# Kernel optimization log

Hardware: AMD Instinct MI355X
Metric: run time of the kernel (lower is better)

Reference implementation:

```python
import jax, jax.numpy as jnp
import numpy as np

B, C, H, W = 8, 256, 64, 64
CQ = C // 8  # q/k projection dim = 32


def setup_inputs() -> dict:
    key = jax.random.key(0)
    ks = jax.random.split(key, 8)
    sq = 1.0 / np.sqrt(C)
    return {
        "x": jax.random.normal(ks[0], (B, C, H, W), dtype=jnp.float32),
        "wq": jax.random.normal(ks[1], (CQ, C), dtype=jnp.float32) * sq,
        "bq": jax.random.normal(ks[2], (CQ,), dtype=jnp.float32) * 0.01,
        "wk": jax.random.normal(ks[3], (CQ, C), dtype=jnp.float32) * sq,
        "bk": jax.random.normal(ks[4], (CQ,), dtype=jnp.float32) * 0.01,
        "wv": jax.random.normal(ks[5], (C, C), dtype=jnp.float32) * sq,
        "bv": jax.random.normal(ks[6], (C,), dtype=jnp.float32) * 0.01,
        "gamma": jax.random.normal(ks[7], (1,), dtype=jnp.float32) * 0.1,
    }


def reference(x, wq, bq, wk, bk, wv, bv, gamma):
    b, c, h, w = x.shape
    n = h * w
    xf = x.reshape(b, c, n)  # [b, C, N] (1x1 conv == channel matmul)
    q = jnp.einsum('oc,bcn->bno', wq, xf) + bq  # [b, N, Cq]
    k = jnp.einsum('oc,bcn->bon', wk, xf) + bk[None, :, None]  # [b, Cq, N]
    v = jnp.einsum('oc,bcn->bon', wv, xf) + bv[None, :, None]  # [b, C, N]
    energy = jnp.einsum('bnq,bqm->bnm', q, k)  # [b, N, N]
    attn = jax.nn.softmax(energy, axis=-1)
    # out[b,c,i] = sum_j v[b,c,j] * attn[b,i,j]  (bmm(v, attn^T))
    out = jnp.einsum('bcj,bij->bci', v, attn).reshape(b, c, h, w)
    return gamma[0] * out + x
```

## Files before the change

kernel.cpp:

```cpp
#include <hip/hip_runtime.h>
#include <hip/hip_bf16.h>
#include <stdint.h>

#define CC 256
#define CQD 32
#define NND 4096

typedef __bf16 bf16x8 __attribute__((ext_vector_type(8)));
typedef float f32x4 __attribute__((ext_vector_type(4)));
typedef float f32x16 __attribute__((ext_vector_type(16)));

__device__ __forceinline__ bf16x8 ld_bf16x8(const __bf16* p) {
    return *reinterpret_cast<const bf16x8*>(p);
}

__global__ __launch_bounds__(256) void prep_weights(
    const float* __restrict__ wq, const float* __restrict__ wk,
    const float* __restrict__ wv, __bf16* __restrict__ wqkb,
    __bf16* __restrict__ wvb) {
    int i = blockIdx.x * 256 + threadIdx.x;
    if (i < 32 * 256) {
        wqkb[i] = (__bf16)wq[i];
    } else if (i < 64 * 256) {
        wqkb[i] = (__bf16)wk[i - 32 * 256];
    } else {
        int j = i - 64 * 256;
        if (j < 256 * 256) wvb[j] = (__bf16)wv[j];
    }
}

__global__ __launch_bounds__(256, 4) void proj_qkv(
    const float* __restrict__ x, const __bf16* __restrict__ wqkb,
    const __bf16* __restrict__ wvb, const float* __restrict__ bq,
    const float* __restrict__ bk, const float* __restrict__ bv,
    __bf16* __restrict__ qb, __bf16* __restrict__ kb,
    __bf16* __restrict__ vb) {
    __shared__ __align__(16) __bf16 xt[32 * 256];
    __shared__ __align__(16) __bf16 wt[320 * 32];

    const int blk = blockIdx.x;
    const int b = blk & 7;
    const int n0 = (blk >> 3) * 32;
    const int tid = threadIdx.x;
    const int lane = tid & 63;
    const int w = tid >> 6;

    const __bf16* wsrc = wqkb + (size_t)(lane >> 2) * CC + (lane & 3) * 8;

#pragma unroll
    for (int i = 0; i < 5; i++) {
        int ins = w * 5 + i;
        __builtin_amdgcn_global_load_lds(
            (const __attribute__((address_space(1))) void*)(wsrc + (size_t)ins * 16 * CC),
            (__attribute__((address_space(3))) void*)(&wt[ins * 512]), 16, 0, 0);
    }

    {
        const int cl = tid >> 3;
        const int ng = tid & 7;
        const float* xrow = x + (size_t)b * CC * NND + n0 + ng * 4;
        f32x4 xv[8];
#pragma unroll
        for (int p = 0; p < 8; p++)
            xv[p] = *reinterpret_cast<const f32x4*>(xrow + (size_t)(p * 32 + cl) * NND);
#pragma unroll
        for (int p = 0; p < 8; p++) {
            int c = p * 32 + cl;
            int c8 = c >> 3;
#pragma unroll
            for (int j = 0; j < 4; j++) {
                int row = ng * 4 + j;
                xt[row * 256 + ((c8 ^ (row & 7)) * 8) + (c & 7)] = (__bf16)xv[p][j];
            }
        }
    }
    __syncthreads();

    const int l15 = lane & 15;
    const int quad = lane >> 4;
    const f32x4 fzero = {0.f, 0.f, 0.f, 0.f};
    f32x4 aqk[2];
    f32x4 av[4][2];
#pragma unroll
    for (int i = 0; i < 2; i++) aqk[i] = fzero;
#pragma unroll
    for (int i = 0; i < 4; i++)
#pragma unroll
        for (int j = 0; j < 2; j++) av[i][j] = fzero;

#pragma unroll
    for (int t = 0; t < 8; t++) {
        const int k0 = t * 32;
        bf16x8 bfx[2];
#pragma unroll
        for (int nt = 0; nt < 2; nt++) {
            int row = nt * 16 + l15;
            int g = (k0 >> 3) + quad;
            bfx[nt] = ld_bf16x8(&xt[row * 256 + ((g ^ (row & 7)) * 8)]);
        }
        bf16x8 aqf = ld_bf16x8(&wt[(w * 16 + l15) * 32 + quad * 8]);
        bf16x8 avf[4];
#pragma unroll
        for (int mt = 0; mt < 4; mt++)
            avf[mt] = ld_bf16x8(&wt[(64 + (w * 4 + mt) * 16 + l15) * 32 + quad * 8]);
        asm volatile("s_waitcnt lgkmcnt(0)" ::: "memory");
        __builtin_amdgcn_s_barrier();
        int kn = (k0 + 32) & 255;
#pragma unroll
        for (int i = 0; i < 5; i++) {
            int ins = w * 5 + i;
            __builtin_amdgcn_global_load_lds(
                (const __attribute__((address_space(1))) void*)(wsrc + (size_t)ins * 16 * CC + kn),
                (__attribute__((address_space(3))) void*)(&wt[ins * 512]), 16, 0, 0);
        }
#pragma unroll
        for (int nt = 0; nt < 2; nt++)
            aqk[nt] = __builtin_amdgcn_mfma_f32_16x16x32_bf16(aqf, bfx[nt], aqk[nt], 0, 0, 0);
#pragma unroll
        for (int mt = 0; mt < 4; mt++)
#pragma unroll
            for (int nt = 0; nt < 2; nt++)
                av[mt][nt] = __builtin_amdgcn_mfma_f32_16x16x32_bf16(avf[mt], bfx[nt], av[mt][nt], 0, 0, 0);
        asm volatile("s_waitcnt vmcnt(0)" ::: "memory");
        __builtin_amdgcn_s_barrier();
    }

    {
        const int ob = (w & 1) * 16 + quad * 4;
        const float* bias = (w < 2) ? bq : bk;
        __bf16* base = (w < 2) ? qb : kb;
#pragma unroll
        for (int nt = 0; nt < 2; nt++) {
            int n = n0 + nt * 16 + l15;
            union { ushort4 u; __bf16 h[4]; } pk;
#pragma unroll
            for (int r = 0; r < 4; r++) pk.h[r] = (__bf16)(aqk[nt][r] + bias[ob + r]);
            *reinterpret_cast<ushort4*>(base + ((size_t)b * NND + n) * CQD + ob) = pk.u;
        }
    }
    __syncthreads();
#pragma unroll
    for (int mt = 0; mt < 4; mt++) {
#pragma unroll
        for (int nt = 0; nt < 2; nt++) {
#pragma unroll
            for (int r = 0; r < 4; r++) {
                int c = (w * 4 + mt) * 16 + quad * 4 + r;
                int nl = nt * 16 + l15;
                xt[c * 32 + (((nl >> 3) ^ (c & 3)) * 8) + (nl & 7)] =
                    (__bf16)(av[mt][nt][r] + bv[c]);
            }
        }
    }
    __syncthreads();
#pragma unroll
    for (int s = 0; s < 4; s++) {
        int c = s * 64 + (tid >> 2);
        int nc = tid & 3;
        bf16x8 vv = ld_bf16x8(&xt[c * 32 + ((nc ^ (c & 3)) * 8)]);
        *reinterpret_cast<bf16x8*>(vb + ((size_t)b * CC + c) * NND + n0 + nc * 8) = vv;
    }
}

__global__ __launch_bounds__(512, 4) void attention(
    const __bf16* __restrict__ qb, const __bf16* __restrict__ kb,
    const __bf16* __restrict__ vb, const float* __restrict__ gamma,
    const float* __restrict__ x, float* __restrict__ out) {
    __shared__ __align__(16) __bf16 Vt[CC * 64];
    __shared__ __align__(16) __bf16 Pt[2][64 * 72];
    __shared__ float lL[2][64];

    const int blk = blockIdx.x;
    const int b = blk & 7;
    const int i0 = (blk >> 3) * 64;
    const int tid = threadIdx.x;
    const int w = tid >> 6;
    const int jh = w >> 2;
    const int iw = w & 3;
    const int lane = tid & 63;
    const int l15 = lane & 15;
    const int quad = lane >> 4;
    const int l31 = lane & 31;
    const int hi = lane >> 5;
    const f32x4 fzero = {0.f, 0.f, 0.f, 0.f};

    bf16x8 qf = ld_bf16x8(qb + ((size_t)b * NND + i0 + iw * 16 + l15) * CQD + quad * 8);

    const __bf16* kbase = kb + ((size_t)b * NND + jh * 32 + l15) * CQD + quad * 8;
    bf16x8 kf[2];
#pragma unroll
    for (int jt = 0; jt < 2; jt++)
        kf[jt] = ld_bf16x8(kbase + (size_t)(jt * 16) * CQD);

    const int vrow = lane >> 3;
    const int vswz = ((lane & 7) ^ vrow) * 8;
    const __bf16* vsrc = vb + ((size_t)(b * CC + w * 32 + vrow)) * NND + vswz;
    __bf16* vdstb = &Vt[(w * 32) * 64];

    f32x16 acc[2];
#pragma unroll
    for (int it = 0; it < 2; it++)
#pragma unroll
        for (int r = 0; r < 16; r++) acc[it][r] = 0.f;
    float l_i = 0.f;

#define ATTN_STEP(J0, BUF)                                                    \
    {                                                                         \
        _Pragma("unroll")                                                     \
        for (int t = 0; t < 4; t++) {                                         \
            __builtin_amdgcn_global_load_lds(                                 \
                (const __attribute__((address_space(1))) void*)(vsrc + (size_t)t * 8 * NND + (J0)), \
                (__attribute__((address_space(3))) void*)(vdstb + t * 8 * 64), 16, 0, 0); \
        }                                                                     \
        __builtin_amdgcn_sched_barrier(0);   \
        f32x4 sT[2];                                                          \
        _Pragma("unroll")                                                     \
        for (int jt = 0; jt < 2; jt++)                                        \
            sT[jt] = __builtin_amdgcn_mfma_f32_16x16x32_bf16(kf[jt], qf, fzero, 0, 0, 0); \
        const int jn = ((J0) + 64) & (NND - 1);                               \
        _Pragma("unroll")                                                     \
        for (int jt = 0; jt < 2; jt++)                                        \
            kf[jt] = ld_bf16x8(kbase + (size_t)(jn + jt * 16) * CQD);         \
        float ps = 0.f;                                                       \
        _Pragma("unroll")                                                     \
        for (int jt = 0; jt < 2; jt++) {                                      \
            union { ushort4 u4; __bf16 h[4]; } pk;                            \
            _Pragma("unroll")                                                 \
            for (int r = 0; r < 4; r++) {                                     \
                float p = __builtin_amdgcn_exp2f(                             \
                    sT[jt][r] * 1.44269504f - 28.85390082f);                  \
                ps += p;                                                      \
                pk.h[r] = (__bf16)p;                                          \
            }                                                                 \
            *reinterpret_cast<ushort4*>(                                      \
                &Pt[BUF][(iw * 16 + l15) * 72 + jh * 32 + jt * 16 + quad * 4]) = pk.u4; \
        }                                                                     \
        l_i += ps;                                                            \
        asm volatile("s_waitcnt lgkmcnt(0)" ::: "memory");                    \
        __builtin_amdgcn_s_barrier();                                         \
        asm volatile("s_waitcnt vmcnt(2)" ::: "memory");                      \
        __builtin_amdgcn_sched_barrier(0);                                    \
        __builtin_amdgcn_s_setprio(1);                                        \
        _Pragma("unroll")                                                     \
        for (int kk = 0; kk < 4; kk++) {                                      \
            int slot = (((kk * 2 + hi) ^ (l31 & 7)) * 8);                     \
            bf16x8 vfrag = ld_bf16x8(&Vt[(w * 32 + l31) * 64 + slot]);        \
            _Pragma("unroll")                                                 \
            for (int it = 0; it < 2; it++) {                                  \
                bf16x8 pfrag = ld_bf16x8(                                     \
                    &Pt[BUF][(it * 32 + l31) * 72 + kk * 16 + hi * 8]);       \
                acc[it] = __builtin_amdgcn_mfma_f32_32x32x16_bf16(            \
                    vfrag, pfrag, acc[it], 0, 0, 0);                          \
            }                                                                 \
        }                                                                     \
        __builtin_amdgcn_s_setprio(0);                                        \
    }

    for (int j0 = 0; j0 < NND; j0 += 128) {
        ATTN_STEP(j0, 0)
        ATTN_STEP(j0 + 64, 1)
    }
#undef ATTN_STEP

    l_i += __shfl_xor(l_i, 16);
    l_i += __shfl_xor(l_i, 32);
    if (quad == 0) lL[jh][iw * 16 + l15] = l_i;
    __syncthreads();
    float g = gamma[0];
#pragma unroll
    for (int it = 0; it < 2; it++) {
        int i = i0 + it * 32 + l31;
        float linv = 1.0f / (lL[0][it * 32 + l31] + lL[1][it * 32 + l31]);
#pragma unroll
        for (int r = 0; r < 16; r++) {
            int c = w * 32 + (r & 3) + 8 * (r >> 2) + 4 * hi;
            size_t off = ((size_t)b * CC + c) * NND + i;
            out[off] = g * (acc[it][r] * linv) + x[off];
        }
    }
}

extern "C" void kernel_launch(void* const* d_in, const int* in_sizes, int n_in,
                              void* d_out, int out_size, void* d_ws, size_t ws_size,
                              hipStream_t stream) {
    const float* x = (const float*)d_in[0];
    const float* wq = (const float*)d_in[1];
    const float* bq = (const float*)d_in[2];
    const float* wk = (const float*)d_in[3];
    const float* bk = (const float*)d_in[4];
    const float* wv = (const float*)d_in[5];
    const float* bv = (const float*)d_in[6];
    const float* gamma = (const float*)d_in[7];
    float* out = (float*)d_out;

    char* ws = (char*)d_ws;
    __bf16* qb = (__bf16*)ws;
    __bf16* kb = (__bf16*)(ws + 2097152);
    __bf16* vb = (__bf16*)(ws + 2 * 2097152);
    __bf16* wqkb = (__bf16*)(ws + 2 * 2097152 + 16777216);
    __bf16* wvb = (__bf16*)(ws + 2 * 2097152 + 16777216 + 32768);

    prep_weights<<<320, 256, 0, stream>>>(wq, wk, wv, wqkb, wvb);
    proj_qkv<<<1024, 256, 0, stream>>>(x, wqkb, wvb, bq, bk, bv, qb, kb, vb);
    attention<<<512, 512, 0, stream>>>(qb, kb, vb, gamma, x, out);
}
```

Before: 203.2 us.

## Software-pipeline attention loop: prefetch next V tile and QK scores across steps

Restructures the attention inner loop so the QK^T MFMA and K fragment load for the next tile are issued before the current PV MFMAs. The V tile global-to-LDS load for the next step is issued only after the current V and P fragments have been read into registers. This overlaps score computation and memory traffic with the PV matrix multiplies, at the cost of more registers for the staged fragments. The projection kernel's block-to-(batch, position) mapping is also changed so consecutive blocks cover the same batch.

```diff
diff --git a/kernel.cpp b/kernel.cpp
--- a/kernel.cpp
+++ b/kernel.cpp
@@ -39,8 +39,8 @@
     __shared__ __align__(16) __bf16 wt[320 * 32];
 
     const int blk = blockIdx.x;
-    const int b = blk & 7;
-    const int n0 = (blk >> 3) * 32;
+    const int b = blk >> 7;
+    const int n0 = (blk & 127) * 32;
     const int tid = threadIdx.x;
     const int lane = tid & 63;
     const int w = tid >> 6;
@@ -204,23 +204,23 @@
         for (int r = 0; r < 16; r++) acc[it][r] = 0.f;
     float l_i = 0.f;
 
+    f32x4 sT[2];
+#pragma unroll
+    for (int jt = 0; jt < 2; jt++)
+        sT[jt] = __builtin_amdgcn_mfma_f32_16x16x32_bf16(kf[jt], qf, fzero, 0, 0, 0);
+#pragma unroll
+    for (int jt = 0; jt < 2; jt++)
+        kf[jt] = ld_bf16x8(kbase + (size_t)(64 + jt * 16) * CQD);
+#pragma unroll
+    for (int t = 0; t < 4; t++) {
+        __builtin_amdgcn_global_load_lds(
+            (const __attribute__((address_space(1))) void*)(vsrc + (size_t)t * 8 * NND),
+            (__attribute__((address_space(3))) void*)(vdstb + t * 8 * 64), 16, 0, 0);
+    }
+
 #define ATTN_STEP(J0, BUF)                                                    \
     {                                                                         \
-        _Pragma("unroll")                                                     \
-        for (int t = 0; t < 4; t++) {                                         \
-            __builtin_amdgcn_global_load_lds(                                 \
-                (const __attribute__((address_space(1))) void*)(vsrc + (size_t)t * 8 * NND + (J0)), \
-                (__attribute__((address_space(3))) void*)(vdstb + t * 8 * 64), 16, 0, 0); \
-        }                                                                     \
-        __builtin_amdgcn_sched_barrier(0);   \
-        f32x4 sT[2];                                                          \
-        _Pragma("unroll")                                                     \
-        for (int jt = 0; jt < 2; jt++)                                        \
-            sT[jt] = __builtin_amdgcn_mfma_f32_16x16x32_bf16(kf[jt], qf, fzero, 0, 0, 0); \
-        const int jn = ((J0) + 64) & (NND - 1);                               \
-        _Pragma("unroll")                                                     \
-        for (int jt = 0; jt < 2; jt++)                                        \
-            kf[jt] = ld_bf16x8(kbase + (size_t)(jn + jt * 16) * CQD);         \
+                         \
         float ps = 0.f;                                                       \
         _Pragma("unroll")                                                     \
         for (int jt = 0; jt < 2; jt++) {                                      \
@@ -238,21 +238,45 @@
         l_i += ps;                                                            \
         asm volatile("s_waitcnt lgkmcnt(0)" ::: "memory");                    \
         __builtin_amdgcn_s_barrier();                                         \
+        __builtin_amdgcn_s_setprio(1);                                        \
+                             \
+        _Pragma("unroll")                                                     \
+        for (int jt = 0; jt < 2; jt++)                                        \
+            sT[jt] = __builtin_amdgcn_mfma_f32_16x16x32_bf16(kf[jt], qf, fzero, 0, 0, 0); \
+        const int jn2 = ((J0) + 128) & (NND - 1);                             \
+        _Pragma("unroll")                                                     \
+        for (int jt = 0; jt < 2; jt++)                                        \
+            kf[jt] = ld_bf16x8(kbase + (size_t)(jn2 + jt * 16) * CQD);        \
+                     \
         asm volatile("s_waitcnt vmcnt(2)" ::: "memory");                      \
         __builtin_amdgcn_sched_barrier(0);                                    \
-        __builtin_amdgcn_s_setprio(1);                                        \
+        bf16x8 vfr[4];                                                        \
+        bf16x8 pfr[8];                                                        \
         _Pragma("unroll")                                                     \
         for (int kk = 0; kk < 4; kk++) {                                      \
             int slot = (((kk * 2 + hi) ^ (l31 & 7)) * 8);                     \
-            bf16x8 vfrag = ld_bf16x8(&Vt[(w * 32 + l31) * 64 + slot]);        \
+            vfr[kk] = ld_bf16x8(&Vt[(w * 32 + l31) * 64 + slot]);             \
             _Pragma("unroll")                                                 \
-            for (int it = 0; it < 2; it++) {                                  \
-                bf16x8 pfrag = ld_bf16x8(                                     \
+            for (int it = 0; it < 2; it++)                                    \
+                pfr[kk * 2 + it] = ld_bf16x8(                                 \
                     &Pt[BUF][(it * 32 + l31) * 72 + kk * 16 + hi * 8]);       \
+        }                                                                     \
+        asm volatile("s_waitcnt lgkmcnt(0)" ::: "memory");                    \
+        __builtin_amdgcn_sched_barrier(0);                                    \
+                 \
+        _Pragma("unroll")                                                     \
+        for (int t = 0; t < 4; t++) {                                         \
+            __builtin_amdgcn_global_load_lds(                                 \
+                (const __attribute__((address_space(1))) void*)(vsrc + (size_t)t * 8 * NND + (((J0) + 64) & (NND - 1))), \
+                (__attribute__((address_space(3))) void*)(vdstb + t * 8 * 64), 16, 0, 0); \
+        }                                                                     \
+        __builtin_amdgcn_sched_barrier(0);                                    \
+        _Pragma("unroll")                                                     \
+        for (int kk = 0; kk < 4; kk++)                                        \
+            _Pragma("unroll")                                                 \
+            for (int it = 0; it < 2; it++)                                    \
                 acc[it] = __builtin_amdgcn_mfma_f32_32x32x16_bf16(            \
-                    vfrag, pfrag, acc[it], 0, 0, 0);                          \
-            }                                                                 \
-        }                                                                     \
+                    vfr[kk], pfr[kk * 2 + it], acc[it], 0, 0, 0);             \
         __builtin_amdgcn_s_setprio(0);                                        \
     }
 
```

Result: no change. 201.0 us (-1.1%).
